# Optimization experiments

Hardware: AMD Instinct MI355X
Metric: run time of the kernel (lower is better)

The kernel has to match this reference:

```python
import jax, jax.numpy as jnp
import numpy as np

B, N, K = 8, 4096, 64          # graphs, nodes per graph, clusters
E_PER = 65536                   # edges per graph (avg degree 16)
EPS = 1e-15


def gcn_conv(x, W, b, src, dst, num_nodes):
    """PyG GCNConv: add self-loops, symmetric deg^-1/2 normalization, sum-aggregate at dst."""
    h = x @ W
    loop = jnp.arange(num_nodes, dtype=src.dtype)
    s_all = jnp.concatenate([src, loop])
    d_all = jnp.concatenate([dst, loop])
    deg = jax.ops.segment_sum(jnp.ones(d_all.shape[0], dtype=h.dtype), d_all, num_segments=num_nodes)
    dis = jnp.where(deg > 0, jax.lax.rsqrt(deg), 0.0)
    msg = h[s_all] * (dis[s_all] * dis[d_all])[:, None]
    return jax.ops.segment_sum(msg, d_all, num_segments=num_nodes) + b


def setup_inputs() -> dict:
    key = jax.random.key(0)
    ks = jax.random.split(key, 12)
    F_in, H, F_out = 128, 128, 128
    x = jax.random.normal(ks[0], (B * N, F_in), dtype=jnp.float32)
    # within-graph random edges, then offset to global node ids
    local = jax.random.randint(ks[1], (2, B * E_PER), 0, N, dtype=jnp.int32)
    offs = jnp.repeat(jnp.arange(B, dtype=jnp.int32) * N, E_PER)
    edge_index = local + offs[None, :]
    batch = jnp.repeat(jnp.arange(B, dtype=jnp.int32), N)

    def lin(k, i, o):
        return (jax.random.normal(k, (i, o), dtype=jnp.float32) / np.float32(np.sqrt(i)))

    return {
        "x": x, "edge_index": edge_index, "batch": batch,
        "W1": lin(ks[2], F_in, H), "b1": jnp.zeros((H,), jnp.float32),
        "W2": lin(ks[3], H, H),    "b2": jnp.zeros((H,), jnp.float32),
        "Wa1": lin(ks[4], H, H),   "ba1": jnp.zeros((H,), jnp.float32),
        "Wa2": lin(ks[5], H, K),   "ba2": jnp.zeros((K,), jnp.float32),
        "Wo": lin(ks[6], H, F_out), "bo": jnp.zeros((F_out,), jnp.float32),
    }


def reference(x, edge_index, batch, W1, b1, W2, b2, Wa1, ba1, Wa2, ba2, Wo, bo):
    num_nodes = B * N
    src, dst = edge_index[0], edge_index[1]
    # two GCN layers (dropout inactive in eval mode)
    h = jax.nn.relu(gcn_conv(x, W1, b1, src, dst, num_nodes))
    h = gcn_conv(h, W2, b2, src, dst, num_nodes)
    # assignment MLP + softmax (module applies softmax; dense_mincut_pool re-applies it)
    s = jax.nn.softmax(jnp.tanh(h @ Wa1 + ba1) @ Wa2 + ba2, axis=-1)
    # to_dense_adj: scatter edges into [B, N, N]
    g = src // N
    adj = jnp.zeros((B, N, N), h.dtype).at[g, src % N, dst % N].add(1.0)
    # to_dense_batch: equal-size graphs -> reshape (mask all True)
    x_d = h.reshape(B, N, -1)
    s_d = jax.nn.softmax(s.reshape(B, N, K), axis=-1)  # PyG internal softmax (double softmax, faithful)
    # dense_mincut_pool
    out = jnp.einsum('bnk,bnf->bkf', s_d, x_d)              # s^T x : [B,K,F]
    As = jnp.einsum('bnm,bmk->bnk', adj, s_d)
    out_adj = jnp.einsum('bnk,bnj->bkj', s_d, As)           # s^T A s : [B,K,K]
    mincut_num = jnp.trace(out_adj, axis1=-2, axis2=-1)
    d_flat = adj.sum(-1)                                    # node degrees
    mincut_den = jnp.einsum('bnk,bn,bnk->b', s_d, d_flat, s_d)  # trace(s^T D s)
    mincut_loss = jnp.mean(-(mincut_num / mincut_den))
    ss = jnp.einsum('bnk,bnj->bkj', s_d, s_d)
    ss_n = jnp.linalg.norm(ss, axis=(-1, -2), keepdims=True)
    i_s = jnp.eye(K, dtype=ss.dtype)
    ortho_loss = jnp.mean(jnp.linalg.norm(ss / ss_n - i_s / jnp.sqrt(jnp.float32(K)), axis=(-1, -2)))
    # zero diagonal + symmetric degree normalization of pooled adj
    out_adj = out_adj * (1.0 - i_s)
    d = jnp.sqrt(out_adj.sum(-1))[:, None, :] + EPS         # [B,1,K]
    out_adj = out_adj / d / jnp.swapaxes(d, 1, 2)
    # output projection
    pooled_x = jax.nn.relu(out.reshape(-1, out.shape[-1]) @ Wo + bo)  # [B*K, F_out]
    pooled_batch = jnp.repeat(jnp.arange(B), K)
    # pooled_adj returned densely: pooled_edge_index == nonzero(pooled_adj > 0) (dynamic shape)
    return pooled_x, out_adj, pooled_batch, mincut_loss, ortho_loss
```

## Files before the change

### kernel.cpp

```cpp
#include <hip/hip_runtime.h>

#define NNODES 32768
#define NEDGES 524288
#define KCL 64
#define CPG 16

typedef _Float16 half8v __attribute__((ext_vector_type(8)));
typedef _Float16 half4v __attribute__((ext_vector_type(4)));
typedef float floatx4 __attribute__((ext_vector_type(4)));

#define WT1_OFF   0
#define WT2_OFF   16384
#define WTA1_OFF  32768
#define WTA2_OFF  49152
#define WTO_OFF   57344
#define WT_TOTAL  73728

__device__ __forceinline__ float wave_sum(float v) {
#pragma unroll
  for (int off = 32; off > 0; off >>= 1) v += __shfl_xor(v, off, 64);
  return v;
}

__global__ __launch_bounds__(256) void hist2_kernel(const int* __restrict__ src, const int* __restrict__ dst,
                                                    int* __restrict__ pIn,
                                                    const float* __restrict__ W1, const float* __restrict__ W2,
                                                    const float* __restrict__ Wa1, const float* __restrict__ Wa2,
                                                    const float* __restrict__ Wo, _Float16* __restrict__ wt16) {
  __shared__ int hIn[4096];
  const int t = threadIdx.x;
  const int g = blockIdx.x >> 4;
  const int ebase = (g << 16) + ((blockIdx.x & 15) << 12);
  const int nbase = g << 12;
  for (int i = t; i < 4096; i += 256) hIn[i] = 0;
  __syncthreads();
  {
    int tg = blockIdx.x * 256 + t;
#pragma unroll
    for (int i = 0; i < 3; i++) {
      int id = tg + i * 32768;
      if (id < WT_TOTAL) {
        const float* W; int base, BN;
        if (id < 16384)      { W = W1;  base = WT1_OFF;  BN = 128; }
        else if (id < 32768) { W = W2;  base = WT2_OFF;  BN = 128; }
        else if (id < 49152) { W = Wa1; base = WTA1_OFF; BN = 128; }
        else if (id < 57344) { W = Wa2; base = WTA2_OFF; BN = 64; }
        else                 { W = Wo;  base = WTO_OFF;  BN = 128; }
        int m = id - base;
        int k = m / BN, n = m % BN;
        wt16[base + n * 128 + k] = (_Float16)W[m];
      }
    }
  }
#pragma unroll
  for (int i = 0; i < 16; ++i) {
    int e = ebase + i * 256 + t;
    atomicAdd(&hIn[dst[e] - nbase], 1);
  }
  __syncthreads();
  int* dIn = pIn + ((size_t)blockIdx.x << 12);
  for (int i = t; i < 4096; i += 256) dIn[i] = hIn[i];
}

__global__ __launch_bounds__(1024) void scan2_kernel(const int* __restrict__ pIn, int* __restrict__ offs,
                                                     int* __restrict__ cbase, float* __restrict__ dis) {
  __shared__ int part[1024];
  const int t = threadIdx.x;
  const int g = blockIdx.x;
  int tot[4];
  int s = 0;
#pragma unroll
  for (int j = 0; j < 4; ++j) {
    int l = t * 4 + j;
    int cnt = 0;
#pragma unroll
    for (int c = 0; c < CPG; ++c) cnt += pIn[(((size_t)(g * CPG + c)) << 12) + l];
    tot[j] = cnt;
    s += cnt;
  }
  part[t] = s;
  __syncthreads();
  for (int off = 1; off < 1024; off <<= 1) {
    int add = (t >= off) ? part[t - off] : 0;
    __syncthreads();
    part[t] += add;
    __syncthreads();
  }
  int run = (g << 16) + ((t == 0) ? 0 : part[t - 1]);
#pragma unroll
  for (int j = 0; j < 4; ++j) {
    int l = t * 4 + j;
    int n = (g << 12) + l;
    offs[n] = run;
    dis[n] = rsqrtf((float)tot[j] + 1.0f);
    int running = run;
#pragma unroll
    for (int c = 0; c < CPG; ++c) {
      size_t idx = (((size_t)(g * CPG + c)) << 12) + l;
      cbase[idx] = running;
      running += pIn[idx];
    }
    run += tot[j];
  }
  if (g == 0 && t == 0) offs[NNODES] = NEDGES;
}

__global__ __launch_bounds__(256) void scatter2_kernel(const int* __restrict__ src, const int* __restrict__ dst,
                                                       const int* __restrict__ cbase, int* __restrict__ ssrc) {
  __shared__ int cur[4096];
  const int t = threadIdx.x;
  const int g = blockIdx.x >> 4;
  const int ebase = (g << 16) + ((blockIdx.x & 15) << 12);
  const int nbase = g << 12;
  const int* cb = cbase + ((size_t)blockIdx.x << 12);
  for (int i = t; i < 4096; i += 256) cur[i] = cb[i];
  __syncthreads();
#pragma unroll
  for (int i = 0; i < 16; ++i) {
    int e = ebase + i * 256 + t;
    int d = dst[e] - nbase;
    int pos = atomicAdd(&cur[d], 1);
    ssrc[pos] = src[e];
  }
}

template <int ACT, int BIAS, int SCALE, int AFP32>
__global__ __launch_bounds__(256) void mgemm_kernel(const void* __restrict__ Ain, const _Float16* __restrict__ WT16,
                                                    const float* __restrict__ bias, const float* __restrict__ rowscale,
                                                    _Float16* __restrict__ Cout) {
  __shared__ _Float16 WT[128][136];
  const int t = threadIdx.x;
#pragma unroll
  for (int i = 0; i < 8; i++) {
    int idx = i * 256 + t;
    int n = idx >> 4, k8 = (idx & 15) << 3;
    *reinterpret_cast<half8v*>(&WT[n][k8]) = *reinterpret_cast<const half8v*>(&WT16[n * 128 + k8]);
  }
  __syncthreads();
  const int lane = t & 63;
  const int quad = lane >> 4, l16 = lane & 15;
  const long rowbase = (long)(blockIdx.x & 7) * 4096 + (long)(blockIdx.x >> 3) * 128 + (t >> 6) * 32;
  half8v af[2][4];
#pragma unroll
  for (int rt = 0; rt < 2; rt++)
#pragma unroll
    for (int kt = 0; kt < 4; kt++) {
      if (AFP32) {
        const float* A32 = (const float*)Ain;
        const float* p = A32 + (rowbase + rt * 16 + l16) * 128 + kt * 32 + quad * 8;
        float4 p0 = *reinterpret_cast<const float4*>(p);
        float4 p1 = *reinterpret_cast<const float4*>(p + 4);
        half8v h = {(_Float16)p0.x, (_Float16)p0.y, (_Float16)p0.z, (_Float16)p0.w,
                    (_Float16)p1.x, (_Float16)p1.y, (_Float16)p1.z, (_Float16)p1.w};
        af[rt][kt] = h;
      } else {
        const _Float16* A16 = (const _Float16*)Ain;
        af[rt][kt] = *reinterpret_cast<const half8v*>(A16 + (rowbase + rt * 16 + l16) * 128 + kt * 32 + quad * 8);
      }
    }
  floatx4 acc[2][8];
#pragma unroll
  for (int rt = 0; rt < 2; rt++)
#pragma unroll
    for (int ct = 0; ct < 8; ct++) acc[rt][ct] = {0.f, 0.f, 0.f, 0.f};
#pragma unroll
  for (int kt = 0; kt < 4; kt++) {
    half8v bf[8];
#pragma unroll
    for (int ct = 0; ct < 8; ct++)
      bf[ct] = *reinterpret_cast<const half8v*>(&WT[ct * 16 + l16][kt * 32 + quad * 8]);
#pragma unroll
    for (int rt = 0; rt < 2; rt++)
#pragma unroll
      for (int ct = 0; ct < 8; ct++)
        acc[rt][ct] = __builtin_amdgcn_mfma_f32_16x16x32_f16(af[rt][kt], bf[ct], acc[rt][ct], 0, 0, 0);
  }
#pragma unroll
  for (int rt = 0; rt < 2; rt++) {
#pragma unroll
    for (int r = 0; r < 4; r++) {
      long row = rowbase + rt * 16 + quad * 4 + r;
      float sc = SCALE ? rowscale[row] : 1.f;
#pragma unroll
      for (int ct = 0; ct < 8; ct++) {
        float v = acc[rt][ct][r];
        if (SCALE) v *= sc;
        if (BIAS) v += bias[ct * 16 + l16];
        if (ACT == 1) v = fmaxf(v, 0.f);
        Cout[row * 128 + ct * 16 + l16] = (_Float16)v;
      }
    }
  }
}

__global__ __launch_bounds__(256) void mlp_kernel(const _Float16* __restrict__ h2, const _Float16* __restrict__ wta1,
                                                  const _Float16* __restrict__ wta2, const float* __restrict__ ba1,
                                                  const float* __restrict__ ba2, _Float16* __restrict__ sh) {
  __shared__ _Float16 WT1[128][136];
  __shared__ _Float16 WT2[64][136];
  __shared__ _Float16 Z[128][136];
  const int t = threadIdx.x;
#pragma unroll
  for (int i = 0; i < 8; i++) {
    int idx = i * 256 + t;
    int n = idx >> 4, k8 = (idx & 15) << 3;
    *reinterpret_cast<half8v*>(&WT1[n][k8]) = *reinterpret_cast<const half8v*>(&wta1[n * 128 + k8]);
  }
#pragma unroll
  for (int i = 0; i < 4; i++) {
    int idx = i * 256 + t;
    int n = idx >> 4, k8 = (idx & 15) << 3;
    *reinterpret_cast<half8v*>(&WT2[n][k8]) = *reinterpret_cast<const half8v*>(&wta2[n * 128 + k8]);
  }
  __syncthreads();
  const int lane = t & 63;
  const int quad = lane >> 4, l16 = lane & 15;
  const int w = t >> 6;
  const long rowbase = (long)(blockIdx.x & 7) * 4096 + (long)(blockIdx.x >> 3) * 128 + w * 32;
  half8v af[2][4];
#pragma unroll
  for (int rt = 0; rt < 2; rt++)
#pragma unroll
    for (int kt = 0; kt < 4; kt++)
      af[rt][kt] = *reinterpret_cast<const half8v*>(h2 + (rowbase + rt * 16 + l16) * 128 + kt * 32 + quad * 8);
  {
    floatx4 acc[2][8];
#pragma unroll
    for (int rt = 0; rt < 2; rt++)
#pragma unroll
      for (int ct = 0; ct < 8; ct++) acc[rt][ct] = {0.f, 0.f, 0.f, 0.f};
#pragma unroll
    for (int kt = 0; kt < 4; kt++) {
      half8v bf[8];
#pragma unroll
      for (int ct = 0; ct < 8; ct++)
        bf[ct] = *reinterpret_cast<const half8v*>(&WT1[ct * 16 + l16][kt * 32 + quad * 8]);
#pragma unroll
      for (int rt = 0; rt < 2; rt++)
#pragma unroll
        for (int ct = 0; ct < 8; ct++)
          acc[rt][ct] = __builtin_amdgcn_mfma_f32_16x16x32_f16(af[rt][kt], bf[ct], acc[rt][ct], 0, 0, 0);
    }
#pragma unroll
    for (int rt = 0; rt < 2; rt++)
#pragma unroll
      for (int r = 0; r < 4; r++) {
        int lrow = w * 32 + rt * 16 + quad * 4 + r;
#pragma unroll
        for (int ct = 0; ct < 8; ct++) {
          float v = tanhf(acc[rt][ct][r] + ba1[ct * 16 + l16]);
          Z[lrow][ct * 16 + l16] = (_Float16)v;
        }
      }
  }
  __syncthreads();
  half8v af2[2][4];
#pragma unroll
  for (int rt = 0; rt < 2; rt++)
#pragma unroll
    for (int kt = 0; kt < 4; kt++)
      af2[rt][kt] = *reinterpret_cast<const half8v*>(&Z[w * 32 + rt * 16 + l16][kt * 32 + quad * 8]);
  floatx4 acc2[2][4];
#pragma unroll
  for (int rt = 0; rt < 2; rt++)
#pragma unroll
    for (int ct = 0; ct < 4; ct++) acc2[rt][ct] = {0.f, 0.f, 0.f, 0.f};
#pragma unroll
  for (int kt = 0; kt < 4; kt++) {
    half8v bf[4];
#pragma unroll
    for (int ct = 0; ct < 4; ct++)
      bf[ct] = *reinterpret_cast<const half8v*>(&WT2[ct * 16 + l16][kt * 32 + quad * 8]);
#pragma unroll
    for (int rt = 0; rt < 2; rt++)
#pragma unroll
      for (int ct = 0; ct < 4; ct++)
        acc2[rt][ct] = __builtin_amdgcn_mfma_f32_16x16x32_f16(af2[rt][kt], bf[ct], acc2[rt][ct], 0, 0, 0);
  }
#pragma unroll
  for (int rt = 0; rt < 2; rt++) {
#pragma unroll
    for (int r = 0; r < 4; r++) {
      long row = rowbase + rt * 16 + quad * 4 + r;
      float v[4];
#pragma unroll
      for (int ct = 0; ct < 4; ct++) v[ct] = acc2[rt][ct][r] + ba2[ct * 16 + l16];
      float m = fmaxf(fmaxf(v[0], v[1]), fmaxf(v[2], v[3]));
#pragma unroll
      for (int off = 1; off <= 8; off <<= 1) m = fmaxf(m, __shfl_xor(m, off, 64));
      float se = 0.f;
#pragma unroll
      for (int ct = 0; ct < 4; ct++) { v[ct] = __expf(v[ct] - m); se += v[ct]; }
#pragma unroll
      for (int off = 1; off <= 8; off <<= 1) se += __shfl_xor(se, off, 64);
      float inv = 1.0f / se;
#pragma unroll
      for (int ct = 0; ct < 4; ct++) v[ct] *= inv;
      float m2 = fmaxf(fmaxf(v[0], v[1]), fmaxf(v[2], v[3]));
#pragma unroll
      for (int off = 1; off <= 8; off <<= 1) m2 = fmaxf(m2, __shfl_xor(m2, off, 64));
      float se2 = 0.f;
#pragma unroll
      for (int ct = 0; ct < 4; ct++) { v[ct] = __expf(v[ct] - m2); se2 += v[ct]; }
#pragma unroll
      for (int off = 1; off <= 8; off <<= 1) se2 += __shfl_xor(se2, off, 64);
      float inv2 = 1.0f / se2;
#pragma unroll
      for (int ct = 0; ct < 4; ct++) sh[row * 64 + ct * 16 + l16] = (_Float16)(v[ct] * inv2);
    }
  }
}

__global__ __launch_bounds__(256) void aggregate_kernel(const _Float16* __restrict__ hs, const float* __restrict__ dis,
                                                        const int* __restrict__ offs, const int* __restrict__ ssrc,
                                                        const float* __restrict__ bias, _Float16* __restrict__ outh,
                                                        int relu) {
  const int lane = threadIdx.x & 63;
  const int b = blockIdx.x;
  const int node = ((b & 7) << 12) + ((b >> 3) << 2) + (threadIdx.x >> 6);
  const int q = lane >> 4;
  const int fl = (lane & 15) * 8;
  const int e0 = offs[node], e1 = offs[node + 1];
  float fa[8];
#pragma unroll
  for (int j = 0; j < 8; j++) fa[j] = 0.f;
  int e = e0;
  for (; e + 16 <= e1; e += 16) {
    int s0 = ssrc[e + q];
    int s1 = ssrc[e + 4 + q];
    int s2 = ssrc[e + 8 + q];
    int s3 = ssrc[e + 12 + q];
    half8v v0 = *reinterpret_cast<const half8v*>(hs + (size_t)s0 * 128 + fl);
    half8v v1 = *reinterpret_cast<const half8v*>(hs + (size_t)s1 * 128 + fl);
    half8v v2 = *reinterpret_cast<const half8v*>(hs + (size_t)s2 * 128 + fl);
    half8v v3 = *reinterpret_cast<const half8v*>(hs + (size_t)s3 * 128 + fl);
#pragma unroll
    for (int j = 0; j < 8; j++) fa[j] += (float)v0[j] + (float)v1[j] + (float)v2[j] + (float)v3[j];
  }
  if (e < e1) {
    int last = e1 - 1;
    int i0 = e + q, i1 = e + 4 + q, i2 = e + 8 + q, i3 = e + 12 + q;
    bool m0 = i0 < e1, m1 = i1 < e1, m2 = i2 < e1, m3 = i3 < e1;
    int s0 = ssrc[i0 < last ? i0 : last];
    int s1 = ssrc[i1 < last ? i1 : last];
    int s2 = ssrc[i2 < last ? i2 : last];
    int s3 = ssrc[i3 < last ? i3 : last];
    half8v v0 = *reinterpret_cast<const half8v*>(hs + (size_t)s0 * 128 + fl);
    half8v v1 = *reinterpret_cast<const half8v*>(hs + (size_t)s1 * 128 + fl);
    half8v v2 = *reinterpret_cast<const half8v*>(hs + (size_t)s2 * 128 + fl);
    half8v v3 = *reinterpret_cast<const half8v*>(hs + (size_t)s3 * 128 + fl);
#pragma unroll
    for (int j = 0; j < 8; j++) {
      fa[j] += (m0 ? (float)v0[j] : 0.f) + (m1 ? (float)v1[j] : 0.f) +
               (m2 ? (float)v2[j] : 0.f) + (m3 ? (float)v3[j] : 0.f);
    }
  }
#pragma unroll
  for (int j = 0; j < 8; j++) {
    fa[j] += __shfl_xor(fa[j], 16, 64);
    fa[j] += __shfl_xor(fa[j], 32, 64);
  }
  if (q == 0) {
    float dn = dis[node];
    half8v self = *reinterpret_cast<const half8v*>(hs + (size_t)node * 128 + fl);
    float4 b0 = *reinterpret_cast<const float4*>(bias + fl);
    float4 b1 = *reinterpret_cast<const float4*>(bias + fl + 4);
    float bb[8] = {b0.x, b0.y, b0.z, b0.w, b1.x, b1.y, b1.z, b1.w};
    half8v r;
#pragma unroll
    for (int j = 0; j < 8; j++) {
      float v = fmaf(fa[j] + (float)self[j], dn, bb[j]);
      if (relu) v = fmaxf(v, 0.f);
      r[j] = (_Float16)v;
    }
    *reinterpret_cast<half8v*>(outh + (size_t)node * 128 + fl) = r;
  }
}

__global__ __launch_bounds__(256) void gather_kernel(const _Float16* __restrict__ sh, const int* __restrict__ offs,
                                                     const int* __restrict__ ssrc, _Float16* __restrict__ Gh,
                                                     float* __restrict__ dnp) {
  const int lane = threadIdx.x & 63;
  const int b = blockIdx.x;
  const int node = ((b & 7) << 12) + ((b >> 3) << 2) + (threadIdx.x >> 6);
  const int q = lane >> 3;
  const int fl = (lane & 7) * 8;
  const int e0 = offs[node], e1 = offs[node + 1];
  float fa[8];
  float sq = 0.f;
#pragma unroll
  for (int j = 0; j < 8; j++) fa[j] = 0.f;
  int e = e0;
  for (; e + 16 <= e1; e += 16) {
    int s0 = ssrc[e + q];
    int s1 = ssrc[e + 8 + q];
    half8v v0 = *reinterpret_cast<const half8v*>(sh + (size_t)s0 * 64 + fl);
    half8v v1 = *reinterpret_cast<const half8v*>(sh + (size_t)s1 * 64 + fl);
#pragma unroll
    for (int j = 0; j < 8; j++) {
      float f0 = (float)v0[j], f1 = (float)v1[j];
      fa[j] += f0 + f1;
      sq = fmaf(f0, f0, sq);
      sq = fmaf(f1, f1, sq);
    }
  }
  if (e < e1) {
    int last = e1 - 1;
    int i0 = e + q, i1 = e + 8 + q;
    bool m0 = i0 < e1, m1 = i1 < e1;
    int s0 = ssrc[i0 < last ? i0 : last];
    int s1 = ssrc[i1 < last ? i1 : last];
    half8v v0 = *reinterpret_cast<const half8v*>(sh + (size_t)s0 * 64 + fl);
    half8v v1 = *reinterpret_cast<const half8v*>(sh + (size_t)s1 * 64 + fl);
#pragma unroll
    for (int j = 0; j < 8; j++) {
      float f0 = m0 ? (float)v0[j] : 0.f;
      float f1 = m1 ? (float)v1[j] : 0.f;
      fa[j] += f0 + f1;
      sq = fmaf(f0, f0, sq);
      sq = fmaf(f1, f1, sq);
    }
  }
#pragma unroll
  for (int j = 0; j < 8; j++) {
    fa[j] += __shfl_xor(fa[j], 8, 64);
    fa[j] += __shfl_xor(fa[j], 16, 64);
    fa[j] += __shfl_xor(fa[j], 32, 64);
  }
  float den = wave_sum(sq);
  if (lane == 0) dnp[node] = den;
  if (q == 0) {
    half8v r;
#pragma unroll
    for (int j = 0; j < 8; j++) r[j] = (_Float16)fa[j];
    *reinterpret_cast<half8v*>(Gh + (size_t)node * 64 + fl) = r;
  }
}

__global__ __launch_bounds__(512) void fused_atb_kernel(const _Float16* __restrict__ sh, const _Float16* __restrict__ Gh,
                                                        const _Float16* __restrict__ h2, float* __restrict__ pF) {
  __shared__ float Xs[32][64];
  __shared__ float Ys[32][256];
  const int t = threadIdx.x;
  const int g = blockIdx.x & 7, chunk = blockIdx.x >> 3;
  const int n0 = g * 4096 + chunk * 128;
  const int rg = t >> 6;
  const int cl = t & 63;
  float acc[8][4];
#pragma unroll
  for (int r = 0; r < 8; r++)
#pragma unroll
    for (int j = 0; j < 4; j++) acc[r][j] = 0.f;

  for (int kt = 0; kt < 4; ++kt) {
    const int nb = n0 + kt * 32;
    {
      int k = t >> 4, c = (t & 15) * 4;
      half4v hv = *reinterpret_cast<const half4v*>(&sh[(size_t)(nb + k) * 64 + c]);
      float4 val = {(float)hv[0], (float)hv[1], (float)hv[2], (float)hv[3]};
      *reinterpret_cast<float4*>(&Xs[k][c]) = val;
    }
#pragma unroll
    for (int it = 0; it < 4; ++it) {
      int slot = it * 512 + t;
      int k = slot >> 6, c = (slot & 63) * 4;
      half4v hv;
      if (c < 64)       hv = *reinterpret_cast<const half4v*>(&Gh[(size_t)(nb + k) * 64 + c]);
      else if (c < 128) hv = *reinterpret_cast<const half4v*>(&sh[(size_t)(nb + k) * 64 + (c - 64)]);
      else              hv = *reinterpret_cast<const half4v*>(&h2[(size_t)(nb + k) * 128 + (c - 128)]);
      float4 val = {(float)hv[0], (float)hv[1], (float)hv[2], (float)hv[3]};
      *reinterpret_cast<float4*>(&Ys[k][c]) = val;
    }
    __syncthreads();
#pragma unroll
    for (int k = 0; k < 32; ++k) {
      float4 b4 = *reinterpret_cast<const float4*>(&Ys[k][cl * 4]);
      float4 a0 = *reinterpret_cast<const float4*>(&Xs[k][rg * 8]);
      float4 a1 = *reinterpret_cast<const float4*>(&Xs[k][rg * 8 + 4]);
      float a[8] = {a0.x, a0.y, a0.z, a0.w, a1.x, a1.y, a1.z, a1.w};
#pragma unroll
      for (int r = 0; r < 8; r++) {
        acc[r][0] = fmaf(a[r], b4.x, acc[r][0]);
        acc[r][1] = fmaf(a[r], b4.y, acc[r][1]);
        acc[r][2] = fmaf(a[r], b4.z, acc[r][2]);
        acc[r][3] = fmaf(a[r], b4.w, acc[r][3]);
      }
    }
    __syncthreads();
  }
  float* dst = pF + (size_t)blockIdx.x * 16384;
#pragma unroll
  for (int r = 0; r < 8; r++) {
    float4 o4 = {acc[r][0], acc[r][1], acc[r][2], acc[r][3]};
    *reinterpret_cast<float4*>(&dst[(rg * 8 + r) * 256 + cl * 4]) = o4;
  }
}

__global__ __launch_bounds__(256) void merge_kernel(const float* __restrict__ pF, float* __restrict__ oadj,
                                                    float* __restrict__ ssb, _Float16* __restrict__ outp16) {
  int idx = blockIdx.x * 256 + threadIdx.x;
  int g = idx >> 12, o4 = idx & 4095;
  float sx = 0.f, sy = 0.f, sz = 0.f, sw = 0.f;
#pragma unroll
  for (int q = 0; q < 32; ++q) {
    float4 v = *reinterpret_cast<const float4*>(pF + (size_t)(q * 8 + g) * 16384 + o4 * 4);
    sx += v.x; sy += v.y; sz += v.z; sw += v.w;
  }
  int row = o4 >> 6;
  int c = (o4 & 63) * 4;
  if (c < 64) {
    float4 o = {sx, sy, sz, sw};
    *reinterpret_cast<float4*>(&oadj[g * 4096 + row * 64 + c]) = o;
  } else if (c < 128) {
    float4 o = {sx, sy, sz, sw};
    *reinterpret_cast<float4*>(&ssb[g * 4096 + row * 64 + (c - 64)]) = o;
  } else {
    half4v h = {(_Float16)sx, (_Float16)sy, (_Float16)sz, (_Float16)sw};
    *reinterpret_cast<half4v*>(&outp16[g * 8192 + row * 128 + (c - 128)]) = h;
  }
}

__global__ __launch_bounds__(256) void epilogue2_kernel(const float* __restrict__ oadj, const float* __restrict__ ssb,
                                                        const _Float16* __restrict__ outp16, const _Float16* __restrict__ wto,
                                                        const float* __restrict__ bo, const float* __restrict__ dn,
                                                        float* __restrict__ out) {
  __shared__ _Float16 outpS[64][136];
  __shared__ _Float16 WoT[128][136];
  __shared__ float red[256];
  __shared__ float rowsum[64];
  __shared__ float dw[4], w1[4], w2[4], w3[4];
  const int g = blockIdx.x, t = threadIdx.x;

#pragma unroll
  for (int i = 0; i < 8; i++) {
    int idx = i * 256 + t;
    int n = idx >> 4, k8 = (idx & 15) << 3;
    *reinterpret_cast<half8v*>(&WoT[n][k8]) = *reinterpret_cast<const half8v*>(&wto[n * 128 + k8]);
  }
#pragma unroll
  for (int i = 0; i < 4; i++) {
    int idx = i * 256 + t;
    int orow = idx >> 4, c8 = (idx & 15) * 8;
    half8v v = *reinterpret_cast<const half8v*>(&outp16[g * 8192 + orow * 128 + c8]);
    *reinterpret_cast<half8v*>(&outpS[orow][c8]) = v;
  }

  const int row = t >> 2, p = t & 3;
  float Areg[16];
  float trs_p = 0.f, ssq_p = 0.f;
#pragma unroll
  for (int c4 = 0; c4 < 4; c4++) {
    float4 a = *reinterpret_cast<const float4*>(&oadj[g * 4096 + row * 64 + p * 16 + c4 * 4]);
    Areg[c4 * 4 + 0] = a.x; Areg[c4 * 4 + 1] = a.y; Areg[c4 * 4 + 2] = a.z; Areg[c4 * 4 + 3] = a.w;
    float4 s = *reinterpret_cast<const float4*>(&ssb[g * 4096 + row * 64 + p * 16 + c4 * 4]);
    float vv[4] = {s.x, s.y, s.z, s.w};
#pragma unroll
    for (int jj = 0; jj < 4; jj++) {
      ssq_p += vv[jj] * vv[jj];
      int col = p * 16 + c4 * 4 + jj;
      if (col == row) trs_p += vv[jj];
    }
  }
  float da = 0.f;
#pragma unroll
  for (int i = 0; i < 16; i++) da += dn[g * 4096 + i * 256 + t];
  float dws = wave_sum(da);
  if ((t & 63) == 0) dw[t >> 6] = dws;

  float rs = 0.f, tra = 0.f;
#pragma unroll
  for (int c = 0; c < 16; c++) {
    int j = p * 16 + c;
    if (j == row) tra += Areg[c];
    else rs += Areg[c];
  }
  red[t] = rs;
  __syncthreads();
  if (p == 0) rowsum[row] = red[t] + red[t + 1] + red[t + 2] + red[t + 3];
  float v1 = wave_sum(tra), v2 = wave_sum(trs_p), v3 = wave_sum(ssq_p);
  if ((t & 63) == 0) { int w = t >> 6; w1[w] = v1; w2[w] = v2; w3[w] = v3; }
  __syncthreads();
  if (t == 0) {
    float TRA = w1[0] + w1[1] + w1[2] + w1[3];
    float TRS = w2[0] + w2[1] + w2[2] + w2[3];
    float SSQ = w3[0] + w3[1] + w3[2] + w3[3];
    float DEN = dw[0] + dw[1] + dw[2] + dw[3];
    atomicAdd(&out[98816], -(TRA / DEN) * 0.125f);
    float ssn = sqrtf(SSQ);
    atomicAdd(&out[98817], sqrtf(2.0f - TRS / (4.0f * ssn)) * 0.125f);
  }
  float di = sqrtf(rowsum[row]) + 1e-15f;
#pragma unroll
  for (int c = 0; c < 16; c++) {
    int j = p * 16 + c;
    float v = (j == row) ? 0.f : Areg[c];
    float dj = sqrtf(rowsum[j]) + 1e-15f;
    out[65536 + g * 4096 + row * 64 + j] = v / (di * dj);
  }
  if (t < 64) out[98304 + g * 64 + t] = (float)g;

  const int lane = t & 63;
  const int quad = lane >> 4, l16 = lane & 15;
  const int w = t >> 6;
  floatx4 acc[8];
#pragma unroll
  for (int ct = 0; ct < 8; ct++) acc[ct] = {0.f, 0.f, 0.f, 0.f};
#pragma unroll
  for (int kt = 0; kt < 4; kt++) {
    half8v af = *reinterpret_cast<const half8v*>(&outpS[w * 16 + l16][kt * 32 + quad * 8]);
#pragma unroll
    for (int ct = 0; ct < 8; ct++) {
      half8v bf = *reinterpret_cast<const half8v*>(&WoT[ct * 16 + l16][kt * 32 + quad * 8]);
      acc[ct] = __builtin_amdgcn_mfma_f32_16x16x32_f16(af, bf, acc[ct], 0, 0, 0);
    }
  }
#pragma unroll
  for (int r = 0; r < 4; r++) {
    int orow = w * 16 + quad * 4 + r;
#pragma unroll
    for (int ct = 0; ct < 8; ct++) {
      int col = ct * 16 + l16;
      float v = fmaxf(acc[ct][r] + bo[col], 0.f);
      out[(g * 64 + orow) * 128 + col] = v;
    }
  }
}

extern "C" void kernel_launch(void* const* d_in, const int* in_sizes, int n_in,
                              void* d_out, int out_size, void* d_ws, size_t ws_size,
                              hipStream_t stream) {
  const float* x   = (const float*)d_in[0];
  const int*   ei  = (const int*)d_in[1];
  const float* W1  = (const float*)d_in[3];
  const float* b1  = (const float*)d_in[4];
  const float* W2  = (const float*)d_in[5];
  const float* b2  = (const float*)d_in[6];
  const float* Wa1 = (const float*)d_in[7];
  const float* ba1 = (const float*)d_in[8];
  const float* Wa2 = (const float*)d_in[9];
  const float* ba2 = (const float*)d_in[10];
  const float* Wo  = (const float*)d_in[11];
  const float* bo  = (const float*)d_in[12];
  const int* src = ei;
  const int* dst = ei + NEDGES;
  float* out = (float*)d_out;

  char* ws = (char*)d_ws;
  size_t o = 0;
  auto alloc = [&](size_t bytes) -> void* {
    void* p = ws + o;
    o += (bytes + 255) & ~(size_t)255;
    return p;
  };
  _Float16* h16A = (_Float16*)alloc((size_t)NNODES * 128 * 2);
  _Float16* h16B = (_Float16*)alloc((size_t)NNODES * 128 * 2);
  _Float16* h16C = (_Float16*)alloc((size_t)NNODES * 128 * 2);
  _Float16* sh   = (_Float16*)alloc((size_t)NNODES * 64 * 2);
  _Float16* Gh   = (_Float16*)alloc((size_t)NNODES * 64 * 2);
  float* pF    = (float*)alloc((size_t)256 * 16384 * 4);
  float* dis   = (float*)alloc((size_t)NNODES * 4);
  int* offs    = (int*)alloc((size_t)(NNODES + 1) * 4);
  int* ssrc    = (int*)alloc((size_t)NEDGES * 4);
  int* pIn     = (int*)alloc((size_t)8 * CPG * 4096 * 4);
  int* cbase   = (int*)alloc((size_t)8 * CPG * 4096 * 4);
  float* dn    = (float*)alloc((size_t)NNODES * 4);
  float* oadj  = (float*)alloc(8 * 4096 * 4);
  float* ssb   = (float*)alloc(8 * 4096 * 4);
  _Float16* outp16 = (_Float16*)alloc(8 * 8192 * 2);
  _Float16* wt16   = (_Float16*)alloc((size_t)WT_TOTAL * 2);

  hipMemsetAsync(out + 98816, 0, 2 * sizeof(float), stream);

  hist2_kernel<<<8 * CPG, 256, 0, stream>>>(src, dst, pIn, W1, W2, Wa1, Wa2, Wo, wt16);
  scan2_kernel<<<8, 1024, 0, stream>>>(pIn, offs, cbase, dis);
  scatter2_kernel<<<8 * CPG, 256, 0, stream>>>(src, dst, cbase, ssrc);

  mgemm_kernel<0, 0, 1, 1><<<NNODES / 128, 256, 0, stream>>>(x, wt16 + WT1_OFF, nullptr, dis, h16A);
  aggregate_kernel<<<NNODES / 4, 256, 0, stream>>>(h16A, dis, offs, ssrc, b1, h16B, 1);
  mgemm_kernel<0, 0, 1, 0><<<NNODES / 128, 256, 0, stream>>>(h16B, wt16 + WT2_OFF, nullptr, dis, h16A);
  aggregate_kernel<<<NNODES / 4, 256, 0, stream>>>(h16A, dis, offs, ssrc, b2, h16C, 0);

  mlp_kernel<<<NNODES / 128, 256, 0, stream>>>(h16C, wt16 + WTA1_OFF, wt16 + WTA2_OFF, ba1, ba2, sh);

  gather_kernel<<<NNODES / 4, 256, 0, stream>>>(sh, offs, ssrc, Gh, dn);
  fused_atb_kernel<<<256, 512, 0, stream>>>(sh, Gh, h16C, pF);
  merge_kernel<<<128, 256, 0, stream>>>(pF, oadj, ssb, outp16);
  epilogue2_kernel<<<8, 256, 0, stream>>>(oadj, ssb, outp16, wt16 + WTO_OFF, bo, dn, out);
}
```

Measured before the change: 216.2 us.

## Fuse assignment gather into ATB kernel, vectorize histogram/scatter, deepen aggregate unroll

Folds the neighbor-sum of assignment rows into the fused s^T A s kernel, keeping the gathered rows in shared memory instead of writing and rereading a global Gh buffer, and drops one kernel launch. The histogram and scatter kernels now read edge indices as int4 and interleave block-to-graph mapping, and the aggregate loop is unrolled to eight outstanding gathers per lane. The risk is reduced parallelism for the gather: 256 blocks of 512 threads now do work previously spread over 8192 blocks, which may expose memory latency. Merge block ordering also changes to interleave graphs.

```diff
diff --git a/kernel.cpp b/kernel.cpp
--- a/kernel.cpp
+++ b/kernel.cpp
@@ -29,8 +29,9 @@
                                                     const float* __restrict__ Wo, _Float16* __restrict__ wt16) {
   __shared__ int hIn[4096];
   const int t = threadIdx.x;
-  const int g = blockIdx.x >> 4;
-  const int ebase = (g << 16) + ((blockIdx.x & 15) << 12);
+  const int g = blockIdx.x & 7;
+  const int chunk = blockIdx.x >> 3;
+  const int ebase = (g << 16) + (chunk << 12);
   const int nbase = g << 12;
   for (int i = t; i < 4096; i += 256) hIn[i] = 0;
   __syncthreads();
@@ -52,13 +53,17 @@
       }
     }
   }
-#pragma unroll
-  for (int i = 0; i < 16; ++i) {
-    int e = ebase + i * 256 + t;
-    atomicAdd(&hIn[dst[e] - nbase], 1);
-  }
-  __syncthreads();
-  int* dIn = pIn + ((size_t)blockIdx.x << 12);
+  const int4* dst4 = reinterpret_cast<const int4*>(dst + ebase);
+#pragma unroll
+  for (int i = 0; i < 4; ++i) {
+    int4 d = dst4[i * 256 + t];
+    atomicAdd(&hIn[d.x - nbase], 1);
+    atomicAdd(&hIn[d.y - nbase], 1);
+    atomicAdd(&hIn[d.z - nbase], 1);
+    atomicAdd(&hIn[d.w - nbase], 1);
+  }
+  __syncthreads();
+  int* dIn = pIn + ((size_t)(g * CPG + chunk) << 12);
   for (int i = t; i < 4096; i += 256) dIn[i] = hIn[i];
 }
 
@@ -109,18 +114,23 @@
                                                        const int* __restrict__ cbase, int* __restrict__ ssrc) {
   __shared__ int cur[4096];
   const int t = threadIdx.x;
-  const int g = blockIdx.x >> 4;
-  const int ebase = (g << 16) + ((blockIdx.x & 15) << 12);
+  const int g = blockIdx.x & 7;
+  const int chunk = blockIdx.x >> 3;
+  const int ebase = (g << 16) + (chunk << 12);
   const int nbase = g << 12;
-  const int* cb = cbase + ((size_t)blockIdx.x << 12);
+  const int* cb = cbase + ((size_t)(g * CPG + chunk) << 12);
   for (int i = t; i < 4096; i += 256) cur[i] = cb[i];
   __syncthreads();
-#pragma unroll
-  for (int i = 0; i < 16; ++i) {
-    int e = ebase + i * 256 + t;
-    int d = dst[e] - nbase;
-    int pos = atomicAdd(&cur[d], 1);
-    ssrc[pos] = src[e];
+  const int4* dst4 = reinterpret_cast<const int4*>(dst + ebase);
+  const int4* src4 = reinterpret_cast<const int4*>(src + ebase);
+#pragma unroll
+  for (int i = 0; i < 4; ++i) {
+    int4 d = dst4[i * 256 + t];
+    int4 s = src4[i * 256 + t];
+    int p0 = atomicAdd(&cur[d.x - nbase], 1); ssrc[p0] = s.x;
+    int p1 = atomicAdd(&cur[d.y - nbase], 1); ssrc[p1] = s.y;
+    int p2 = atomicAdd(&cur[d.z - nbase], 1); ssrc[p2] = s.z;
+    int p3 = atomicAdd(&cur[d.w - nbase], 1); ssrc[p3] = s.w;
   }
 }
 
@@ -325,34 +335,33 @@
 #pragma unroll
   for (int j = 0; j < 8; j++) fa[j] = 0.f;
   int e = e0;
-  for (; e + 16 <= e1; e += 16) {
-    int s0 = ssrc[e + q];
-    int s1 = ssrc[e + 4 + q];
-    int s2 = ssrc[e + 8 + q];
-    int s3 = ssrc[e + 12 + q];
-    half8v v0 = *reinterpret_cast<const half8v*>(hs + (size_t)s0 * 128 + fl);
-    half8v v1 = *reinterpret_cast<const half8v*>(hs + (size_t)s1 * 128 + fl);
-    half8v v2 = *reinterpret_cast<const half8v*>(hs + (size_t)s2 * 128 + fl);
-    half8v v3 = *reinterpret_cast<const half8v*>(hs + (size_t)s3 * 128 + fl);
-#pragma unroll
-    for (int j = 0; j < 8; j++) fa[j] += (float)v0[j] + (float)v1[j] + (float)v2[j] + (float)v3[j];
+  for (; e + 32 <= e1; e += 32) {
+    int s[8];
+#pragma unroll
+    for (int jj = 0; jj < 8; jj++) s[jj] = ssrc[e + jj * 4 + q];
+#pragma unroll
+    for (int jj = 0; jj < 8; jj++) {
+      half8v v = *reinterpret_cast<const half8v*>(hs + (size_t)s[jj] * 128 + fl);
+#pragma unroll
+      for (int j = 0; j < 8; j++) fa[j] += (float)v[j];
+    }
   }
   if (e < e1) {
     int last = e1 - 1;
-    int i0 = e + q, i1 = e + 4 + q, i2 = e + 8 + q, i3 = e + 12 + q;
-    bool m0 = i0 < e1, m1 = i1 < e1, m2 = i2 < e1, m3 = i3 < e1;
-    int s0 = ssrc[i0 < last ? i0 : last];
-    int s1 = ssrc[i1 < last ? i1 : last];
-    int s2 = ssrc[i2 < last ? i2 : last];
-    int s3 = ssrc[i3 < last ? i3 : last];
-    half8v v0 = *reinterpret_cast<const half8v*>(hs + (size_t)s0 * 128 + fl);
-    half8v v1 = *reinterpret_cast<const half8v*>(hs + (size_t)s1 * 128 + fl);
-    half8v v2 = *reinterpret_cast<const half8v*>(hs + (size_t)s2 * 128 + fl);
-    half8v v3 = *reinterpret_cast<const half8v*>(hs + (size_t)s3 * 128 + fl);
-#pragma unroll
-    for (int j = 0; j < 8; j++) {
-      fa[j] += (m0 ? (float)v0[j] : 0.f) + (m1 ? (float)v1[j] : 0.f) +
-               (m2 ? (float)v2[j] : 0.f) + (m3 ? (float)v3[j] : 0.f);
+    int s[8]; bool m[8];
+#pragma unroll
+    for (int jj = 0; jj < 8; jj++) {
+      int idx = e + jj * 4 + q;
+      m[jj] = idx < e1;
+      s[jj] = ssrc[idx < last ? idx : last];
+    }
+#pragma unroll
+    for (int jj = 0; jj < 8; jj++) {
+      half8v v = *reinterpret_cast<const half8v*>(hs + (size_t)s[jj] * 128 + fl);
+      if (m[jj]) {
+#pragma unroll
+        for (int j = 0; j < 8; j++) fa[j] += (float)v[j];
+      }
     }
   }
 #pragma unroll
@@ -377,75 +386,86 @@
   }
 }
 
-__global__ __launch_bounds__(256) void gather_kernel(const _Float16* __restrict__ sh, const int* __restrict__ offs,
-                                                     const int* __restrict__ ssrc, _Float16* __restrict__ Gh,
-                                                     float* __restrict__ dnp) {
-  const int lane = threadIdx.x & 63;
-  const int b = blockIdx.x;
-  const int node = ((b & 7) << 12) + ((b >> 3) << 2) + (threadIdx.x >> 6);
-  const int q = lane >> 3;
-  const int fl = (lane & 7) * 8;
-  const int e0 = offs[node], e1 = offs[node + 1];
-  float fa[8];
-  float sq = 0.f;
-#pragma unroll
-  for (int j = 0; j < 8; j++) fa[j] = 0.f;
-  int e = e0;
-  for (; e + 16 <= e1; e += 16) {
-    int s0 = ssrc[e + q];
-    int s1 = ssrc[e + 8 + q];
-    half8v v0 = *reinterpret_cast<const half8v*>(sh + (size_t)s0 * 64 + fl);
-    half8v v1 = *reinterpret_cast<const half8v*>(sh + (size_t)s1 * 64 + fl);
-#pragma unroll
-    for (int j = 0; j < 8; j++) {
-      float f0 = (float)v0[j], f1 = (float)v1[j];
-      fa[j] += f0 + f1;
-      sq = fmaf(f0, f0, sq);
-      sq = fmaf(f1, f1, sq);
-    }
-  }
-  if (e < e1) {
-    int last = e1 - 1;
-    int i0 = e + q, i1 = e + 8 + q;
-    bool m0 = i0 < e1, m1 = i1 < e1;
-    int s0 = ssrc[i0 < last ? i0 : last];
-    int s1 = ssrc[i1 < last ? i1 : last];
-    half8v v0 = *reinterpret_cast<const half8v*>(sh + (size_t)s0 * 64 + fl);
-    half8v v1 = *reinterpret_cast<const half8v*>(sh + (size_t)s1 * 64 + fl);
-#pragma unroll
-    for (int j = 0; j < 8; j++) {
-      float f0 = m0 ? (float)v0[j] : 0.f;
-      float f1 = m1 ? (float)v1[j] : 0.f;
-      fa[j] += f0 + f1;
-      sq = fmaf(f0, f0, sq);
-      sq = fmaf(f1, f1, sq);
-    }
-  }
-#pragma unroll
-  for (int j = 0; j < 8; j++) {
-    fa[j] += __shfl_xor(fa[j], 8, 64);
-    fa[j] += __shfl_xor(fa[j], 16, 64);
-    fa[j] += __shfl_xor(fa[j], 32, 64);
-  }
-  float den = wave_sum(sq);
-  if (lane == 0) dnp[node] = den;
-  if (q == 0) {
-    half8v r;
-#pragma unroll
-    for (int j = 0; j < 8; j++) r[j] = (_Float16)fa[j];
-    *reinterpret_cast<half8v*>(Gh + (size_t)node * 64 + fl) = r;
-  }
-}
-
-__global__ __launch_bounds__(512) void fused_atb_kernel(const _Float16* __restrict__ sh, const _Float16* __restrict__ Gh,
-                                                        const _Float16* __restrict__ h2, float* __restrict__ pF) {
+__global__ __launch_bounds__(512) void fused_atb_kernel(const _Float16* __restrict__ sh, const _Float16* __restrict__ h2,
+                                                        const int* __restrict__ offs, const int* __restrict__ ssrc,
+                                                        float* __restrict__ dnp, float* __restrict__ pF) {
   __shared__ float Xs[32][64];
   __shared__ float Ys[32][256];
+  __shared__ _Float16 Gs[128][64];
   const int t = threadIdx.x;
   const int g = blockIdx.x & 7, chunk = blockIdx.x >> 3;
   const int n0 = g * 4096 + chunk * 128;
-  const int rg = t >> 6;
-  const int cl = t & 63;
+  const int w = t >> 6;
+  const int lane = t & 63;
+
+  {
+    const int q = lane >> 3;
+    const int fl = (lane & 7) * 8;
+    for (int i = 0; i < 16; ++i) {
+      const int node = n0 + w * 16 + i;
+      const int e0 = offs[node], e1 = offs[node + 1];
+      float fa[8];
+      float sq = 0.f;
+#pragma unroll
+      for (int j = 0; j < 8; j++) fa[j] = 0.f;
+      int e = e0;
+      for (; e + 32 <= e1; e += 32) {
+        int s[4];
+#pragma unroll
+        for (int jj = 0; jj < 4; jj++) s[jj] = ssrc[e + jj * 8 + q];
+#pragma unroll
+        for (int jj = 0; jj < 4; jj++) {
+          half8v v = *reinterpret_cast<const half8v*>(sh + (size_t)s[jj] * 64 + fl);
+#pragma unroll
+          for (int j = 0; j < 8; j++) {
+            float f = (float)v[j];
+            fa[j] += f;
+            sq = fmaf(f, f, sq);
+          }
+        }
+      }
+      if (e < e1) {
+        int last = e1 - 1;
+        int s[4]; bool m[4];
+#pragma unroll
+        for (int jj = 0; jj < 4; jj++) {
+          int idx = e + jj * 8 + q;
+          m[jj] = idx < e1;
+          s[jj] = ssrc[idx < last ? idx : last];
+        }
+#pragma unroll
+        for (int jj = 0; jj < 4; jj++) {
+          half8v v = *reinterpret_cast<const half8v*>(sh + (size_t)s[jj] * 64 + fl);
+          if (m[jj]) {
+#pragma unroll
+            for (int j = 0; j < 8; j++) {
+              float f = (float)v[j];
+              fa[j] += f;
+              sq = fmaf(f, f, sq);
+            }
+          }
+        }
+      }
+#pragma unroll
+      for (int j = 0; j < 8; j++) {
+        fa[j] += __shfl_xor(fa[j], 8, 64);
+        fa[j] += __shfl_xor(fa[j], 16, 64);
+        fa[j] += __shfl_xor(fa[j], 32, 64);
+      }
+      float den = wave_sum(sq);
+      if (lane == 0) dnp[node] = den;
+      if (q == 0) {
+        half8v r;
+#pragma unroll
+        for (int j = 0; j < 8; j++) r[j] = (_Float16)fa[j];
+        *reinterpret_cast<half8v*>(&Gs[w * 16 + i][fl]) = r;
+      }
+    }
+  }
+  __syncthreads();
+
+  const int rg = w;
+  const int cl = lane;
   float acc[8][4];
 #pragma unroll
   for (int r = 0; r < 8; r++)
@@ -465,7 +485,7 @@
       int slot = it * 512 + t;
       int k = slot >> 6, c = (slot & 63) * 4;
       half4v hv;
-      if (c < 64)       hv = *reinterpret_cast<const half4v*>(&Gh[(size_t)(nb + k) * 64 + c]);
+      if (c < 64)       hv = *reinterpret_cast<const half4v*>(&Gs[kt * 32 + k][c]);
       else if (c < 128) hv = *reinterpret_cast<const half4v*>(&sh[(size_t)(nb + k) * 64 + (c - 64)]);
       else              hv = *reinterpret_cast<const half4v*>(&h2[(size_t)(nb + k) * 128 + (c - 128)]);
       float4 val = {(float)hv[0], (float)hv[1], (float)hv[2], (float)hv[3]};
@@ -498,8 +518,8 @@
 
 __global__ __launch_bounds__(256) void merge_kernel(const float* __restrict__ pF, float* __restrict__ oadj,
                                                     float* __restrict__ ssb, _Float16* __restrict__ outp16) {
-  int idx = blockIdx.x * 256 + threadIdx.x;
-  int g = idx >> 12, o4 = idx & 4095;
+  int g = blockIdx.x & 7;
+  int o4 = (blockIdx.x >> 3) * 256 + threadIdx.x;
   float sx = 0.f, sy = 0.f, sz = 0.f, sw = 0.f;
 #pragma unroll
   for (int q = 0; q < 32; ++q) {
@@ -656,7 +676,6 @@
   _Float16* h16B = (_Float16*)alloc((size_t)NNODES * 128 * 2);
   _Float16* h16C = (_Float16*)alloc((size_t)NNODES * 128 * 2);
   _Float16* sh   = (_Float16*)alloc((size_t)NNODES * 64 * 2);
-  _Float16* Gh   = (_Float16*)alloc((size_t)NNODES * 64 * 2);
   float* pF    = (float*)alloc((size_t)256 * 16384 * 4);
   float* dis   = (float*)alloc((size_t)NNODES * 4);
   int* offs    = (int*)alloc((size_t)(NNODES + 1) * 4);
@@ -682,8 +701,7 @@
 
   mlp_kernel<<<NNODES / 128, 256, 0, stream>>>(h16C, wt16 + WTA1_OFF, wt16 + WTA2_OFF, ba1, ba2, sh);
 
-  gather_kernel<<<NNODES / 4, 256, 0, stream>>>(sh, offs, ssrc, Gh, dn);
-  fused_atb_kernel<<<256, 512, 0, stream>>>(sh, Gh, h16C, pF);
+  fused_atb_kernel<<<256, 512, 0, stream>>>(sh, h16C, offs, ssrc, dn, pF);
   merge_kernel<<<128, 256, 0, stream>>>(pF, oadj, ssb, outp16);
   epilogue2_kernel<<<8, 256, 0, stream>>>(oadj, ssb, outp16, wt16 + WTO_OFF, bo, dn, out);
 }
```

New measurement: 227.1 us. 1.05x slower.
